# Kernel optimization log

Hardware: AMD Instinct MI355X
Metric: run time of the kernel (lower is better)

## Reference

```python
import jax, jax.numpy as jnp
import numpy as np

K, PS, WS, WT, NHEADS, STRIDE0_A, STRIDE0 = 7, 7, 8, 1, 1, 8, 4
SCALE = STRIDE0_A // STRIDE0  # index-upsampling factor (coarse stride 8 -> fine stride 4)


def _reflect(i, L):
    # dnls-style reflect bounds: i<0 -> -i, i>=L -> 2*(L-1)-i (single reflection suffices here)
    i = jnp.abs(i)
    return jnp.where(i >= L, 2 * (L - 1) - i, i)


def _patch_offsets(ps):
    pr = jnp.arange(ps) - ps // 2
    return jnp.stack(jnp.meshgrid(pr, pr, indexing='ij'), -1).reshape(-1, 2)  # [ps*ps, 2]


def _exact_search(vid0, vid1):
    # coarse windowed patch-product k-NN search (prod_with_heads), stride0_a query grid
    B, T, C, H, W = vid0.shape
    HD, Ch = NHEADS, C // NHEADS
    v0 = jnp.moveaxis(vid0, 2, -1)  # [B,T,H,W,C]
    v1 = jnp.moveaxis(vid1, 2, -1)
    nH, nW = H // STRIDE0_A, W // STRIDE0_A
    qt, qi, qj = [a.reshape(-1) for a in jnp.meshgrid(jnp.arange(T), jnp.arange(nH), jnp.arange(nW), indexing='ij')]
    qh, qw = qi * STRIDE0_A, qj * STRIDE0_A
    Q = qt.shape[0]
    st = 2 * WT + 1  # temporal window, shifted to stay in [0,T)
    t0 = jnp.clip(qt - WT, 0, T - st)
    offs = jnp.arange(WS) - WS // 2  # spatial window offsets, stride1=1
    ct = jnp.broadcast_to((t0[:, None] + jnp.arange(st))[:, :, None, None], (Q, st, WS, WS)).reshape(Q, -1)
    ch = jnp.broadcast_to((qh[:, None] + offs)[:, None, :, None], (Q, st, WS, WS)).reshape(Q, -1)
    cw = jnp.broadcast_to((qw[:, None] + offs)[:, None, None, :], (Q, st, WS, WS)).reshape(Q, -1)
    S = st * WS * WS
    poffs = _patch_offsets(PS)

    def body(acc, off):  # accumulate patch inner products one patch-pixel at a time (memory-light)
        dr, dc = off[0], off[1]
        p0 = v0[:, qt, _reflect(qh + dr, H), _reflect(qw + dc, W)]   # [B,Q,C]
        p1 = v1[:, ct, _reflect(ch + dr, H), _reflect(cw + dc, W)]   # [B,Q,S,C]
        d = jnp.einsum('bqnc,bqsnc->bnqs', p0.reshape(B, Q, HD, Ch), p1.reshape(B, Q, S, HD, Ch))
        return acc + d, None

    dists, _ = jax.lax.scan(jax.checkpoint(body), jnp.zeros((B, HD, Q, S), v0.dtype), poffs)
    vals, idx = jax.lax.top_k(dists, K)  # product search -> largest first
    qsel = jnp.arange(Q)[None, None, :, None]
    inds = jnp.stack([ct[qsel, idx], ch[qsel, idx], cw[qsel, idx]], -1)  # [B,HD,Q,K,3]
    return vals, inds


def _upsample_inds(inds_a, T, H, W):
    # interpolate_inds: replicate coarse inds to the fine stride0 grid, shifted by the
    # fine-query offset relative to its parent coarse query; anchor self at slot 0.
    nH, nW = H // STRIDE0_A, W // STRIDE0_A
    nHf, nWf = H // STRIDE0, W // STRIDE0
    ft, fi, fj = [a.reshape(-1) for a in jnp.meshgrid(jnp.arange(T), jnp.arange(nHf), jnp.arange(nWf), indexing='ij')]
    fh, fw = fi * STRIDE0, fj * STRIDE0
    ci = jnp.clip(fi // SCALE, 0, nH - 1)
    cj = jnp.clip(fj // SCALE, 0, nW - 1)
    qlin = ft * nH * nW + ci * nW + cj
    base = inds_a[:, :, qlin]  # [B,HD,Qf,K,3]
    dh = (fh - ci * STRIDE0_A)[None, None, :, None]
    dw = (fw - cj * STRIDE0_A)[None, None, :, None]
    it = base[..., 0]
    ih = _reflect(base[..., 1] + dh, H)
    iw = _reflect(base[..., 2] + dw, W)
    it = it.at[..., 0].set(ft[None, None, :])  # anchor_self=True
    ih = ih.at[..., 0].set(fh[None, None, :])
    iw = iw.at[..., 0].set(fw[None, None, :])
    return (ft, fh, fw), (it, ih, iw)


def _refine_dists(vid0, vid1, fq, cand):
    # prod_refine with ws_r=1: evaluate the patch product exactly at the given inds
    B, T, C, H, W = vid0.shape
    HD, Ch = NHEADS, C // NHEADS
    ft, fh, fw = fq
    it, ih, iw = cand
    Qf, k = it.shape[2], it.shape[3]
    v0 = jnp.moveaxis(vid0, 2, -1)                                # [B,T,H,W,C]
    v1h = jnp.moveaxis(vid1, 2, -1).reshape(B, T, H, W, HD, Ch)
    bidx = jnp.arange(B)[:, None, None, None]
    hidx = jnp.arange(HD)[None, :, None, None]
    poffs = _patch_offsets(PS)

    def body(acc, off):
        dr, dc = off[0], off[1]
        p0 = v0[:, ft, _reflect(fh + dr, H), _reflect(fw + dc, W)]              # [B,Qf,C]
        p1 = v1h[bidx, it, _reflect(ih + dr, H), _reflect(iw + dc, W), hidx]    # [B,HD,Qf,k,Ch]
        d = jnp.einsum('bqnc,bnqkc->bnqk', p0.reshape(B, Qf, HD, Ch), p1)
        return acc + d, None

    dists, _ = jax.lax.scan(jax.checkpoint(body), jnp.zeros((B, HD, Qf, k), v0.dtype), poffs)
    return dists


def setup_inputs() -> dict:
    key = jax.random.key(0)
    k0, k1 = jax.random.split(key)
    B, T, C, H, W = 1, 3, 64, 192, 192
    vid0 = jax.random.normal(k0, (B, T, C, H, W), dtype=jnp.float32)
    vid1 = jax.random.normal(k1, (B, T, C, H, W), dtype=jnp.float32)
    flows = jnp.zeros((B, T, 2, H, W), dtype=jnp.float32)  # accepted but unused (fflow/bflow=None)
    return {"vid0": vid0, "vid1": vid1, "flows": flows}


def reference(vid0, vid1, flows):
    B, T, C, H, W = vid0.shape
    dists_a, inds_a = _exact_search(vid0, vid1)            # coarse stride0_a search
    fq, cand = _upsample_inds(inds_a, T, H, W)             # interpolate inds to stride0 grid
    dists_f = _refine_dists(vid0, vid1, fq, cand)          # refine (fill) dists at fine inds
    inds_f = jnp.stack(cand, -1)                           # [B,HD,Qf,K,3]
    return dists_f, inds_f
```

## Files before the change

### kernel.cpp

```cpp
#include <hip/hip_runtime.h>
#include <math.h>

#define TT   3
#define CC   64
#define HH   192
#define WW   192
#define HWW  (HH*WW)
#define NHC  24
#define NWC  24
#define QC   1728
#define SC   192
#define NPIX 49
#define KK   7
#define NHF  48
#define NWF  48
#define QF   6912

__device__ __forceinline__ int reflect(int i, int L) {
  i = i < 0 ? -i : i;
  return (i >= L) ? (2 * (L - 1) - i) : i;
}

__global__ void transpose_tchw_thwc(const float* __restrict__ in0,
                                    const float* __restrict__ in1,
                                    float* __restrict__ out0,
                                    float* __restrict__ out1) {
  const float* in = blockIdx.y ? in1 : in0;
  float* out = blockIdx.y ? out1 : out0;
  int b = blockIdx.x;
  int x0 = (b % 3) * 64;
  int ty = b / 3;
  int t = ty / HH, y = ty % HH;

  __shared__ float tile[64][65];
  int lx = threadIdx.x & 63;
  int lc = threadIdx.x >> 6;

  const float* src = in + (size_t)t * CC * HWW + (size_t)y * WW + x0;
#pragma unroll
  for (int i = 0; i < 16; ++i) {
    int c = lc + i * 4;
    tile[c][lx] = src[(size_t)c * HWW + lx];
  }
  __syncthreads();
  float* dst = out + ((size_t)(t * HH + y) * WW + x0) * CC;
#pragma unroll
  for (int i = 0; i < 16; ++i) {
    int x = lc + i * 4;
    dst[(size_t)x * CC + lx] = tile[lx][x];
  }
}

__global__ __launch_bounds__(256, 4) void coarse_fma_kernel(
    const float* __restrict__ v0, const float* __restrict__ v1,
    int* __restrict__ topk) {
  int bid = blockIdx.x;
  int q = (bid & 7) * (QC / 8) + (bid >> 3);
  int qt = q / (NHC * NWC);
  int r = q % (NHC * NWC);
  int qh = (r / NWC) * 8;
  int qw = (r % NWC) * 8;

  __shared__ float4 region4[4 * 196];
  __shared__ float4 qbuf4[16 * 49];
  __shared__ float  dall[SC];
  float* wbuf = (float*)region4;

  int tid = threadIdx.x;
  int s = tid & 63;
  int w = tid >> 6;
  int oi = s >> 3, oj = s & 7;

  int pxb[13];
#pragma unroll
  for (int i = 0; i < 13; ++i) {
    int p = w + 4 * i;
    if (p > 48) p = 48;
    pxb[i] = ((oi + p / 7) * 14 + (oj + p % 7)) * 16;
  }

  {
    const float* b0 = v0 + (size_t)qt * HWW * CC;
    for (int idx = tid; idx < 896; idx += 256) {
      int p = (idx & 7) | ((idx >> 7) << 3);
      int c4 = (idx >> 3) & 15;
      if (p < 49) {
        int ry = reflect(qh + p / 7 - 3, HH);
        int rx = reflect(qw + p % 7 - 3, WW);
        qbuf4[c4 * 49 + p] = *reinterpret_cast<const float4*>(
            b0 + ((size_t)ry * WW + rx) * CC + c4 * 4);
      }
    }
  }

  float4 rr0, rr1, rr2, rr3;
  int src0, src1, src2, src3;
#define SLOT_SRC(j, srcv)                                                   \
  {                                                                         \
    int idx = tid + 256 * (j);                                              \
    int px = (idx & 7) | ((idx >> 5) << 3);                                 \
    int c4h = (idx >> 3) & 3;                                               \
    int ry = reflect(qh - 7 + px / 14, HH);                                 \
    int rx = reflect(qw - 7 + px % 14, WW);                                 \
    srcv = (ry * WW + rx) * CC + c4h * 4;   \
  }
  SLOT_SRC(0, src0) SLOT_SRC(1, src1) SLOT_SRC(2, src2) SLOT_SRC(3, src3)
#undef SLOT_SRC

#define ISSUE(nb)                                                           \
  {                                                                         \
    rr0 = *reinterpret_cast<const float4*>((nb) + src0);                    \
    rr1 = *reinterpret_cast<const float4*>((nb) + src1);                    \
    rr2 = *reinterpret_cast<const float4*>((nb) + src2);                    \
    rr3 = *reinterpret_cast<const float4*>((nb) + src3);                    \
  }
#define WRITE_SLOT(j, rrv)                                                  \
  {                                                                         \
    int idx = tid + 256 * (j);                                              \
    int px = (idx & 7) | ((idx >> 5) << 3);                                 \
    int c4h = (idx >> 3) & 3;                                               \
    if (px < 196) region4[c4h * 196 + px] = rrv;                            \
  }
#define WRITE_ALL                                                           \
  WRITE_SLOT(0, rr0) WRITE_SLOT(1, rr1) WRITE_SLOT(2, rr2) WRITE_SLOT(3, rr3)

  ISSUE(v1)

  for (int ct = 0; ct < 3; ++ct) {
    const float* b1 = v1 + (size_t)ct * HWW * CC;
    float acc[13];
#pragma unroll
    for (int i = 0; i < 13; ++i) acc[i] = 0.f;

#pragma unroll
    for (int ph = 0; ph < 4; ++ph) {
      __syncthreads();
      WRITE_ALL
      __syncthreads();
      const float* nb = (ph < 3) ? (b1 + (ph + 1) * 16)
                                 : ((ct < 2) ? (b1 + (size_t)HWW * CC) : b1);
      ISSUE(nb)

#pragma unroll
      for (int i = 0; i < 13; ++i) {
        if (i < 12 || w == 0) {
          int p = w + 4 * i;
          const char* rbase = reinterpret_cast<const char*>(region4) + pxb[i];
#pragma unroll
          for (int c4h = 0; c4h < 4; ++c4h) {
            float4 a = qbuf4[(ph * 4 + c4h) * 49 + p];
            float4 b = *reinterpret_cast<const float4*>(rbase + c4h * 3136);
            acc[i] = fmaf(a.x, b.x, acc[i]);
            acc[i] = fmaf(a.y, b.y, acc[i]);
            acc[i] = fmaf(a.z, b.z, acc[i]);
            acc[i] = fmaf(a.w, b.w, acc[i]);
          }
        }
      }
    }

    __syncthreads();
#pragma unroll
    for (int i = 0; i < 13; ++i) {
      if (i < 12 || w == 0) wbuf[s * 49 + (w + 4 * i)] = acc[i];
    }
    __syncthreads();
    if (tid < 64) {
      float a = 0.f;
      const float* wr = wbuf + tid * 49;
      for (int p = 0; p < NPIX; ++p)
        a = __fadd_rn(a, wr[p]);
      dall[ct * 64 + tid] = a;
    }
  }
#undef ISSUE
#undef WRITE_SLOT
#undef WRITE_ALL

  __syncthreads();
  if (tid < 64) {
    int lane = tid;
    float va = dall[lane], vb = dall[lane + 64], vc = dall[lane + 128];
    int tk = 0;
#pragma unroll
    for (int k = 0; k < KK; ++k) {
      float bv = -INFINITY;
      int bi = 0x7fffffff;
      if (!(tk & 1) && va > bv) { bv = va; bi = lane; }
      if (!(tk & 2) && vb > bv) { bv = vb; bi = lane + 64; }
      if (!(tk & 4) && vc > bv) { bv = vc; bi = lane + 128; }
#pragma unroll
      for (int off = 32; off > 0; off >>= 1) {
        float ov = __shfl_xor(bv, off, 64);
        int oi2 = __shfl_xor(bi, off, 64);
        if (ov > bv || (ov == bv && oi2 < bi)) { bv = ov; bi = oi2; }
      }
      if ((bi & 63) == lane) tk |= 1 << (bi >> 6);
      if (lane == 0) topk[q * KK + k] = bi;
    }
  }
}

__global__ __launch_bounds__(448, 7) void refine_kernel(
    const float* __restrict__ v0, const float* __restrict__ v1,
    const int* __restrict__ topk, float* __restrict__ out) {
  int bid = blockIdx.x;
  int f = (bid & 7) * (QF / 8) + (bid >> 3);
  int ft = f / (NHF * NWF);
  int r = f % (NHF * NWF);
  int fi = r / NWF, fj = r % NWF;
  int fh = fi * 4, fw = fj * 4;
  int ci = fi >> 1, cj = fj >> 1;
  int dh = (fi & 1) * 4, dw = (fj & 1) * 4;
  int qlin = ft * (NHC * NWC) + ci * NWC + cj;

  int tid = threadIdx.x;
  int lane = tid & 63;
  int k = tid >> 6;

  __shared__ float qs[NPIX * CC];

  {
    const float* b0 = v0 + (size_t)ft * HWW * CC;
#pragma unroll
    for (int i = 0; i < 7; ++i) {
      int idx = tid + i * 448;
      int p = idx >> 6, c = idx & 63;
      int ry = reflect(fh + p / 7 - 3, HH);
      int rx = reflect(fw + p % 7 - 3, WW);
      qs[idx] = b0[((size_t)ry * WW + rx) * CC + c];
    }
  }
  __syncthreads();

  int it, ih, iw;
  if (k == 0) {
    it = ft; ih = fh; iw = fw;
  } else {
    int s = topk[qlin * KK + k];
    int ti = s >> 6;
    int oi = (s >> 3) & 7, oj = s & 7;
    it = ti;
    ih = reflect(ci * 8 + oi - 4 + dh, HH);
    iw = reflect(cj * 8 + oj - 4 + dw, WW);
  }

  const float* b1 = v1 + (size_t)it * HWW * CC;
  float acc = 0.f;
#pragma unroll
  for (int pr = 0; pr < 7; ++pr) {
    int ry = reflect(ih + pr - 3, HH);
    const float* rowp = b1 + (size_t)ry * WW * CC + lane;
    float vals[7];
#pragma unroll
    for (int pc = 0; pc < 7; ++pc) {
      int rx = reflect(iw + pc - 3, WW);
      vals[pc] = rowp[(size_t)rx * CC];
    }
#pragma unroll
    for (int pc = 0; pc < 7; ++pc)
      acc = fmaf(qs[(pr * 7 + pc) * CC + lane], vals[pc], acc);
  }
#pragma unroll
  for (int off = 32; off > 0; off >>= 1)
    acc += __shfl_xor(acc, off, 64);
  if (lane == 0) {
    float* dout = out;
    float* iout = out + (size_t)QF * KK;
    dout[(size_t)f * KK + k] = acc;
    float* ip = iout + ((size_t)f * KK + k) * 3;
    ip[0] = (float)it;
    ip[1] = (float)ih;
    ip[2] = (float)iw;
  }
}

extern "C" void kernel_launch(void* const* d_in, const int* in_sizes, int n_in,
                              void* d_out, int out_size, void* d_ws,
                              size_t ws_size, hipStream_t stream) {
  const float* vid0 = (const float*)d_in[0];
  const float* vid1 = (const float*)d_in[1];
  float* out = (float*)d_out;

  char* ws = (char*)d_ws;
  int* topk = (int*)ws;
  size_t off = (size_t)QC * KK * sizeof(int);
  off = (off + 255) & ~(size_t)255;
  float* v0t = (float*)(ws + off);
  size_t vbytes = (size_t)TT * HWW * CC * sizeof(float);
  float* v1t = (float*)(ws + off + vbytes);

  transpose_tchw_thwc<<<dim3(TT * HH * (WW / 64), 2), 256, 0, stream>>>(
      vid0, vid1, v0t, v1t);
  coarse_fma_kernel<<<QC, 256, 0, stream>>>(v0t, v1t, topk);
  refine_kernel<<<QF, 448, 0, stream>>>(v0t, v1t, topk, out);
}
```

Measured before the change: 268.3 us.

## Remap refine kernel to half-wave per neighbor with vectorized float2/float4 loads

The refine kernel now gives each of the 7 neighbors half a wavefront (32 lanes, two channels each) instead of a full 64-lane wave, so blocks shrink from 448 to 256 threads. The query patch is staged into shared memory with float4 loads, and the candidate patch reads use float2. This is meant to cut thread count and per-thread load instructions and to shorten the shuffle reduction. It adds one idle half-wave (a duplicated neighbor whose result is masked out) and uses more registers per thread.

```diff
diff --git a/kernel.cpp b/kernel.cpp
--- a/kernel.cpp
+++ b/kernel.cpp
@@ -201,7 +201,7 @@
   }
 }
 
-__global__ __launch_bounds__(448, 7) void refine_kernel(
+__global__ __launch_bounds__(256, 8) void refine_kernel(
     const float* __restrict__ v0, const float* __restrict__ v1,
     const int* __restrict__ topk, float* __restrict__ out) {
   int bid = blockIdx.x;
@@ -216,28 +216,32 @@
 
   int tid = threadIdx.x;
   int lane = tid & 63;
-  int k = tid >> 6;
+  int wv = tid >> 6;
+  int hf = lane >> 5;
+  int cl = lane & 31;
+  int k = 2 * wv + hf;
+  int kk = (k < 7) ? k : 6;
 
   __shared__ float qs[NPIX * CC];
 
   {
     const float* b0 = v0 + (size_t)ft * HWW * CC;
-#pragma unroll
-    for (int i = 0; i < 7; ++i) {
-      int idx = tid + i * 448;
-      int p = idx >> 6, c = idx & 63;
+    float4* qs4 = reinterpret_cast<float4*>(qs);
+    for (int idx = tid; idx < 784; idx += 256) {
+      int p = idx >> 4, c4 = idx & 15;
       int ry = reflect(fh + p / 7 - 3, HH);
       int rx = reflect(fw + p % 7 - 3, WW);
-      qs[idx] = b0[((size_t)ry * WW + rx) * CC + c];
+      qs4[idx] = *reinterpret_cast<const float4*>(
+          b0 + ((size_t)ry * WW + rx) * CC + c4 * 4);
     }
   }
   __syncthreads();
 
   int it, ih, iw;
-  if (k == 0) {
+  if (kk == 0) {
     it = ft; ih = fh; iw = fw;
   } else {
-    int s = topk[qlin * KK + k];
+    int s = topk[qlin * KK + kk];
     int ti = s >> 6;
     int oi = (s >> 3) & 7, oj = s & 7;
     it = ti;
@@ -246,25 +250,30 @@
   }
 
   const float* b1 = v1 + (size_t)it * HWW * CC;
-  float acc = 0.f;
+  const float2* qs2 = reinterpret_cast<const float2*>(qs);
+  float accx = 0.f, accy = 0.f;
 #pragma unroll
   for (int pr = 0; pr < 7; ++pr) {
     int ry = reflect(ih + pr - 3, HH);
-    const float* rowp = b1 + (size_t)ry * WW * CC + lane;
-    float vals[7];
+    const float* rowp = b1 + (size_t)ry * WW * CC + 2 * cl;
+    float2 vals[7];
 #pragma unroll
     for (int pc = 0; pc < 7; ++pc) {
       int rx = reflect(iw + pc - 3, WW);
-      vals[pc] = rowp[(size_t)rx * CC];
-    }
-#pragma unroll
-    for (int pc = 0; pc < 7; ++pc)
-      acc = fmaf(qs[(pr * 7 + pc) * CC + lane], vals[pc], acc);
-  }
-#pragma unroll
-  for (int off = 32; off > 0; off >>= 1)
+      vals[pc] = *reinterpret_cast<const float2*>(rowp + (size_t)rx * CC);
+    }
+#pragma unroll
+    for (int pc = 0; pc < 7; ++pc) {
+      float2 a = qs2[(pr * 7 + pc) * 32 + cl];
+      accx = fmaf(a.x, vals[pc].x, accx);
+      accy = fmaf(a.y, vals[pc].y, accy);
+    }
+  }
+  float acc = accx + accy;
+#pragma unroll
+  for (int off = 16; off > 0; off >>= 1)
     acc += __shfl_xor(acc, off, 64);
-  if (lane == 0) {
+  if (cl == 0 && k < 7) {
     float* dout = out;
     float* iout = out + (size_t)QF * KK;
     dout[(size_t)f * KK + k] = acc;
@@ -293,5 +302,5 @@
   transpose_tchw_thwc<<<dim3(TT * HH * (WW / 64), 2), 256, 0, stream>>>(
       vid0, vid1, v0t, v1t);
   coarse_fma_kernel<<<QC, 256, 0, stream>>>(v0t, v1t, topk);
-  refine_kernel<<<QF, 448, 0, stream>>>(v0t, v1t, topk, out);
-}
+  refine_kernel<<<QF, 256, 0, stream>>>(v0t, v1t, topk, out);
+}
```

Result: slower. 285.1 us (+6.3%).
